# Optimization experiments

Hardware: AMD Instinct MI355X
Metric: run time of the kernel (lower is better)

## Reference

```python
import jax, jax.numpy as jnp
import numpy as np

N = 65536          # total nodes across batch
C = 256            # in channels
COUT = 256         # out channels
B = 8              # batch size (graphs)
EMB = 512          # emb channels
N_EDGE_TYPE = 7
N_NODE_TYPE = 7
AVG_DEGREE = 7
E = N * AVG_DEGREE
GROUP = 32         # min(32, channels)
EPS = 1e-5


def setup_inputs() -> dict:
    key = jax.random.key(0)
    ks = jax.random.split(key, 10)
    # GraphConv init: uniform xavier-like with fan scaled by avg_degree
    std = (2.0 / float(AVG_DEGREE * C + AVG_DEGREE * COUT)) ** 0.5
    a = (3.0 ** 0.5) * std
    return {
        "x": jax.random.normal(ks[0], (N, C), jnp.float32),
        "emb": jax.random.normal(ks[1], (B, EMB), jnp.float32),
        "batch_id": jnp.sort(jax.random.randint(ks[2], (N,), 0, B, jnp.int32)),
        "edge_index": jax.random.randint(ks[3], (2, E), 0, N, jnp.int32),
        "edge_type": jax.random.randint(ks[4], (E,), 0, N_EDGE_TYPE, jnp.int32),
        "node_type": jax.random.randint(ks[5], (N,), 0, N_NODE_TYPE, jnp.int32),
        "gn1_w": jnp.ones((1, C), jnp.float32),
        "gn1_b": jnp.zeros((1, C), jnp.float32),
        "conv1_w": jax.random.uniform(ks[6], (N_EDGE_TYPE * (C + N_NODE_TYPE), COUT), jnp.float32, -a, a),
        "emb_w": jax.random.normal(ks[7], (EMB, COUT), jnp.float32) * 0.02,
        "emb_b": jnp.zeros((COUT,), jnp.float32),
        "gn2_w": jnp.ones((1, COUT), jnp.float32),
        "gn2_b": jnp.zeros((1, COUT), jnp.float32),
        "conv2_w": jax.random.uniform(ks[8], (N_EDGE_TYPE * (COUT + N_NODE_TYPE), COUT), jnp.float32, -a, a),
    }


def _adjust_for_group(t, cpg):
    # sum stats within each group of cpg channels, broadcast back: [B, C]
    if cpg > 1:
        Bsz, Cn = t.shape
        g = Cn // cpg
        t = t.reshape(Bsz, g, cpg).sum(-1, keepdims=True)
        t = jnp.broadcast_to(t, (Bsz, g, cpg)).reshape(Bsz, Cn)
    return t


def dual_octree_group_norm(data, batch_id, w, b):
    # data: [N, C]; per-graph group norm via segment sums
    Cn = data.shape[1]
    cpg = Cn // GROUP
    ones = jnp.ones((data.shape[0], 1), data.dtype)
    count = jax.ops.segment_sum(ones, batch_id, num_segments=B) * cpg   # [B,1]
    inv_count = 1.0 / (count + EPS)
    mean = jax.ops.segment_sum(data, batch_id, num_segments=B) * inv_count
    mean = _adjust_for_group(mean, cpg)
    out = data - mean[batch_id]
    var = jax.ops.segment_sum(out * out, batch_id, num_segments=B) * inv_count
    var = _adjust_for_group(var, cpg)
    inv_std = 1.0 / jnp.sqrt(var + EPS)
    out = out * inv_std[batch_id]
    return out * w + b


def graph_conv(x, weights, edge_index, edge_type, node_type):
    # concat one-hot node type channels
    one_hot = jax.nn.one_hot(node_type, N_NODE_TYPE, dtype=x.dtype)
    xa = jnp.concatenate([x, one_hot], axis=1)          # [N, C+T]
    row, col = edge_index[0], edge_index[1]
    index = row * N_EDGE_TYPE + edge_type               # [E]
    col_data = jax.ops.segment_sum(xa[col], index, num_segments=xa.shape[0] * N_EDGE_TYPE)
    return col_data.reshape(xa.shape[0], -1) @ weights  # [N, COUT]


def reference(x, emb, batch_id, edge_index, edge_type, node_type,
              gn1_w, gn1_b, conv1_w, emb_w, emb_b, gn2_w, gn2_b, conv2_w):
    h = dual_octree_group_norm(x, batch_id, gn1_w, gn1_b)
    h = jax.nn.silu(h)
    h = graph_conv(h, conv1_w, edge_index, edge_type, node_type)
    emb_out = jax.nn.silu(emb) @ emb_w + emb_b          # [B, COUT]
    h = h + emb_out[batch_id]                           # per-batch add (loop in torch)
    h = dual_octree_group_norm(h, batch_id, gn2_w, gn2_b)
    h = jax.nn.silu(h)                                  # dropout p=0 -> identity
    h = graph_conv(h, conv2_w, edge_index, edge_type, node_type)
    return x + h                                        # skip is Identity (Cout==C)
```

## Files before the change

kernel.cpp:

```cpp
#include <hip/hip_runtime.h>
#include <math.h>

#define N_NODES 65536
#define B_GR    8
#define EMB_N   512
#define E_EDGES 458752
#define NSEG    458752
#define TSTRIDE 288
#define GK      2016
#define EPS     1e-5f

typedef unsigned short u16;
typedef unsigned int   u32;
typedef __bf16 bf16x8 __attribute__((ext_vector_type(8)));
typedef float  f32x4  __attribute__((ext_vector_type(4)));
typedef u16    u16x8  __attribute__((ext_vector_type(8)));

__device__ __forceinline__ float bf2f(u16 u) {
    u32 x = ((u32)u) << 16; float f; __builtin_memcpy(&f, &x, 4); return f;
}
__device__ __forceinline__ u16 f2bf(float f) {
    u32 x; __builtin_memcpy(&x, &f, 4);
    u32 r = x + 0x7fffu + ((x >> 16) & 1u);
    return (u16)(r >> 16);
}

#define SW(row, k8) ((k8) ^ (((row) >> 1) & 3))

__global__ __launch_bounds__(256) void zero_kernel(int* __restrict__ hist,
                                                   float* __restrict__ S, float* __restrict__ Q) {
    int i = blockIdx.x * 256 + threadIdx.x;
    if (i < NSEG) hist[i] = 0;
    if (i < 2048) { S[i] = 0.f; Q[i] = 0.f; }
}
__global__ __launch_bounds__(256) void zero_sq_kernel(float* __restrict__ S, float* __restrict__ Q) {
    int i = blockIdx.x * 256 + threadIdx.x;
    if (i < 2048) { S[i] = 0.f; Q[i] = 0.f; }
}

__global__ __launch_bounds__(256) void prep_kernel(
    const float* __restrict__ w1, const float* __restrict__ w2,
    u16* __restrict__ Wt1, u16* __restrict__ Wt2,
    const float* __restrict__ emb, const float* __restrict__ embw,
    const float* __restrict__ embb, float* __restrict__ embout)
{
    int bid = blockIdx.x, tid = threadIdx.x;
    if (bid < 4032) {
        const float* Win = (bid < 2016) ? w1 : w2;
        u16* Wt = (bid < 2016) ? Wt1 : Wt2;
        int idx = (bid % 2016) * 256 + tid;
        int n = idx / GK;
        int k = idx - n * GK;
        int t = k / TSTRIDE;
        int c = k - t * TSTRIDE;
        u16 v = (c < 263) ? f2bf(Win[(size_t)(t * 263 + c) * 256 + n]) : (u16)0;
        Wt[idx] = v;
    } else {
        __shared__ float semb[B_GR * EMB_N];
        for (int i = tid; i < B_GR * EMB_N; i += 256) {
            float e = emb[i];
            semb[i] = e / (1.f + expf(-e));
        }
        __syncthreads();
        float acc[8];
        float bb = embb[tid];
#pragma unroll
        for (int b = 0; b < 8; b++) acc[b] = bb;
        for (int k = 0; k < EMB_N; k++) {
            float wv = embw[k * 256 + tid];
#pragma unroll
            for (int b = 0; b < 8; b++) acc[b] += semb[b * EMB_N + k] * wv;
        }
#pragma unroll
        for (int b = 0; b < 8; b++) embout[b * 256 + tid] = acc[b];
    }
}

__global__ __launch_bounds__(256) void stats_kernel(const float* __restrict__ xin,
                                                    const int* __restrict__ batch_id,
                                                    float* __restrict__ S, float* __restrict__ Q) {
    int c = threadIdx.x;
    int n0 = blockIdx.x * 64;
    float s = 0.f, q = 0.f;
    int bcur = batch_id[n0];
    for (int r = 0; r < 64; r++) {
        int n = n0 + r;
        int b = batch_id[n];
        if (b != bcur) {
            atomicAdd(&S[bcur * 256 + c], s);
            atomicAdd(&Q[bcur * 256 + c], q);
            s = 0.f; q = 0.f; bcur = b;
        }
        float v = xin[(size_t)n * 256 + c];
        s += v;
        q = fmaf(v, v, q);
    }
    atomicAdd(&S[bcur * 256 + c], s);
    atomicAdd(&Q[bcur * 256 + c], q);
}

__global__ __launch_bounds__(256) void finalize_kernel(const int* __restrict__ batch_id,
                                                       const float* __restrict__ S, const float* __restrict__ Q,
                                                       float* __restrict__ gmean, float* __restrict__ gistd) {
    __shared__ int scnt[8];
    int tid = threadIdx.x;
    if (tid < 8) scnt[tid] = 0;
    __syncthreads();
    int c0=0,c1=0,c2=0,c3=0,c4=0,c5=0,c6=0,c7=0;
    for (int i = tid; i < N_NODES; i += 256) {
        int b = batch_id[i];
        c0 += (b==0); c1 += (b==1); c2 += (b==2); c3 += (b==3);
        c4 += (b==4); c5 += (b==5); c6 += (b==6); c7 += (b==7);
    }
    atomicAdd(&scnt[0], c0); atomicAdd(&scnt[1], c1); atomicAdd(&scnt[2], c2); atomicAdd(&scnt[3], c3);
    atomicAdd(&scnt[4], c4); atomicAdd(&scnt[5], c5); atomicAdd(&scnt[6], c6); atomicAdd(&scnt[7], c7);
    __syncthreads();
    int b = tid >> 5, g = tid & 31;
    float Sg = 0.f, Qg = 0.f;
#pragma unroll
    for (int k = 0; k < 8; k++) {
        Sg += S[b * 256 + g * 8 + k];
        Qg += Q[b * 256 + g * 8 + k];
    }
    float cnt8 = (float)scnt[b] * 8.f;
    float D = cnt8 + EPS;
    float m = Sg / D;
    float var = (Qg - 2.f * m * Sg + cnt8 * m * m) / D;
    float istd = rsqrtf(var + EPS);
    gmean[tid] = m;
    gistd[tid] = istd;
}

__global__ __launch_bounds__(256) void norm_silu_kernel(const float* __restrict__ xin,
                                                        const int* __restrict__ batch_id,
                                                        const float* __restrict__ gmean, const float* __restrict__ gistd,
                                                        const float* __restrict__ w, const float* __restrict__ bias,
                                                        u16* __restrict__ yout) {
    int tid = threadIdx.x;
    int n = blockIdx.x * 8 + (tid >> 5);
    int g = tid & 31;
    int c0 = g * 8;
    int b = batch_id[n];
    float m = gmean[b * 32 + g], is = gistd[b * 32 + g];
    u16x8 o;
#pragma unroll
    for (int k = 0; k < 8; k++) {
        float v = (xin[(size_t)n * 256 + c0 + k] - m) * is;
        v = v * w[c0 + k] + bias[c0 + k];
        v = v / (1.f + expf(-v));
        o[k] = f2bf(v);
    }
    *(u16x8*)&yout[(size_t)n * 256 + c0] = o;
}

__global__ __launch_bounds__(256) void hist_kernel(const int* __restrict__ ei, const int* __restrict__ et,
                                                   int* __restrict__ hist) {
    int e = blockIdx.x * 256 + threadIdx.x;
    if (e >= E_EDGES) return;
    int s = ei[e] * 7 + et[e];
    atomicAdd(&hist[s], 1);
}

__global__ __launch_bounds__(512) void scan1_kernel(const int* __restrict__ hist, int* __restrict__ partials) {
    __shared__ int sd[512];
    int i = blockIdx.x * 512 + threadIdx.x;
    sd[threadIdx.x] = hist[i];
    __syncthreads();
    for (int off = 256; off > 0; off >>= 1) {
        if (threadIdx.x < off) sd[threadIdx.x] += sd[threadIdx.x + off];
        __syncthreads();
    }
    if (threadIdx.x == 0) partials[blockIdx.x] = sd[0];
}

__global__ __launch_bounds__(1024) void scan2_kernel(int* __restrict__ partials) {
    __shared__ int sd[1024];
    int t = threadIdx.x;
    int v = (t < 896) ? partials[t] : 0;
    sd[t] = v;
    __syncthreads();
    for (int off = 1; off < 1024; off <<= 1) {
        int u = (t >= off) ? sd[t - off] : 0;
        __syncthreads();
        sd[t] += u;
        __syncthreads();
    }
    if (t < 896) partials[t] = sd[t] - v;
}

__global__ __launch_bounds__(512) void scan3_kernel(int* __restrict__ hist_offs, const int* __restrict__ partials,
                                                    int* __restrict__ cursor) {
    __shared__ int sd[512];
    int t = threadIdx.x;
    int i = blockIdx.x * 512 + t;
    int c = hist_offs[i];
    sd[t] = c;
    __syncthreads();
    for (int off = 1; off < 512; off <<= 1) {
        int u = (t >= off) ? sd[t - off] : 0;
        __syncthreads();
        sd[t] += u;
        __syncthreads();
    }
    int o = partials[blockIdx.x] + sd[t] - c;
    hist_offs[i] = o;
    cursor[i] = o;
}

__global__ __launch_bounds__(256) void fill_kernel(const int* __restrict__ ei, const int* __restrict__ et,
                                                   int* __restrict__ cursor, int* __restrict__ elist) {
    int e = blockIdx.x * 256 + threadIdx.x;
    if (e >= E_EDGES) return;
    int s = ei[e] * 7 + et[e];
    int p = atomicAdd(&cursor[s], 1);
    if (p >= 0 && p < E_EDGES) elist[p] = ei[E_EDGES + e];
}

__global__ __launch_bounds__(256) void gemm_fused_kernel(
    const u16* __restrict__ y, const u16* __restrict__ Bt,
    const int* __restrict__ offs, const int* __restrict__ cursor,
    const int* __restrict__ elist, const int* __restrict__ node_type,
    const int* __restrict__ batch_id, const float* __restrict__ embout,
    const float* __restrict__ xres, float* __restrict__ out, int mode)
{
    __shared__ __align__(16) u16 As[64 * 32];
    __shared__ __align__(16) u16 Bs[256 * 32];
    int tid = threadIdx.x;
    int lane = tid & 63;
    int wn = tid >> 6;
    int lm = lane & 15, lq = lane >> 4;
    int m0 = blockIdx.x * 64;
    int ar = tid >> 2, aq = tid & 3;

    f32x4 acc[4][4];
    f32x4 zz = {0.f, 0.f, 0.f, 0.f};
#pragma unroll
    for (int i = 0; i < 4; i++)
#pragma unroll
        for (int j = 0; j < 4; j++) acc[i][j] = zz;

    const u16* btp = Bt + (size_t)ar * GK + aq * 8;

    float a8[8];
    u16x8 breg[4];

    for (int t = 0; t < 7; t++) {
        int s = (m0 + ar) * 7 + t;
        int st = offs[s], en = cursor[s];
        int cnt = en - st;
        int col[4];
#pragma unroll
        for (int u = 0; u < 4; u++) col[u] = (cnt > u) ? elist[st + u] : -1;

#pragma unroll
        for (int j = 0; j < 8; j++) a8[j] = 0.f;
        {
            int cb = aq * 8;
#pragma unroll
            for (int u = 0; u < 4; u++)
                if (col[u] >= 0) {
                    u16x8 v = *(const u16x8*)&y[(size_t)col[u] * 256 + cb];
#pragma unroll
                    for (int j = 0; j < 8; j++) a8[j] += bf2f(v[j]);
                }
            if (cnt > 4)
                for (int e = st + 4; e < en; e++) {
                    u16x8 v = *(const u16x8*)&y[(size_t)elist[e] * 256 + cb];
#pragma unroll
                    for (int j = 0; j < 8; j++) a8[j] += bf2f(v[j]);
                }
        }
        {
            int kb = t * TSTRIDE;
#pragma unroll
            for (int i2 = 0; i2 < 4; i2++) breg[i2] = *(const u16x8*)&btp[(size_t)i2 * 64 * GK + kb];
        }

#pragma unroll
        for (int c9 = 0; c9 < 9; c9++) {
            __syncthreads();
            u16x8 o;
#pragma unroll
            for (int j = 0; j < 8; j++) o[j] = f2bf(a8[j]);
            *(u16x8*)&As[ar * 32 + SW(ar, aq) * 8] = o;
#pragma unroll
            for (int i2 = 0; i2 < 4; i2++) {
                int row = ar + i2 * 64;
                *(u16x8*)&Bs[row * 32 + SW(row, aq) * 8] = breg[i2];
            }
            __syncthreads();
            bf16x8 a[4], b[4];
#pragma unroll
            for (int i = 0; i < 4; i++) {
                int ra = i * 16 + lm;
                a[i] = *(const bf16x8*)&As[ra * 32 + SW(ra, lq) * 8];
            }
#pragma unroll
            for (int j = 0; j < 4; j++) {
                int rb = wn * 64 + j * 16 + lm;
                b[j] = *(const bf16x8*)&Bs[rb * 32 + SW(rb, lq) * 8];
            }
            u16x8 gv[4];
            int nt4[4];
#pragma unroll
            for (int j = 0; j < 8; j++) a8[j] = 0.f;
            if (c9 < 7) {
                int cb = (c9 + 1) * 32 + aq * 8;
#pragma unroll
                for (int u = 0; u < 4; u++)
                    if (col[u] >= 0) gv[u] = *(const u16x8*)&y[(size_t)col[u] * 256 + cb];
                int kb = t * TSTRIDE + (c9 + 1) * 32;
#pragma unroll
                for (int i2 = 0; i2 < 4; i2++) breg[i2] = *(const u16x8*)&btp[(size_t)i2 * 64 * GK + kb];
            } else if (c9 == 7) {
                if (aq == 0) {
#pragma unroll
                    for (int u = 0; u < 4; u++)
                        if (col[u] >= 0) nt4[u] = node_type[col[u]];
                }
                int kb = t * TSTRIDE + 8 * 32;
#pragma unroll
                for (int i2 = 0; i2 < 4; i2++) breg[i2] = *(const u16x8*)&btp[(size_t)i2 * 64 * GK + kb];
            }
#pragma unroll
            for (int i = 0; i < 4; i++)
#pragma unroll
                for (int j = 0; j < 4; j++)
                    acc[i][j] = __builtin_amdgcn_mfma_f32_16x16x32_bf16(a[i], b[j], acc[i][j], 0, 0, 0);
            if (c9 < 7) {
#pragma unroll
                for (int u = 0; u < 4; u++)
                    if (col[u] >= 0) {
#pragma unroll
                        for (int j = 0; j < 8; j++) a8[j] += bf2f(gv[u][j]);
                    }
                if (cnt > 4) {
                    int cb = (c9 + 1) * 32 + aq * 8;
                    for (int e = st + 4; e < en; e++) {
                        u16x8 v = *(const u16x8*)&y[(size_t)elist[e] * 256 + cb];
#pragma unroll
                        for (int j = 0; j < 8; j++) a8[j] += bf2f(v[j]);
                    }
                }
            } else if (c9 == 7) {
                if (aq == 0) {
#pragma unroll
                    for (int u = 0; u < 4; u++)
                        if (col[u] >= 0) {
#pragma unroll
                            for (int j = 0; j < 7; j++) a8[j] += (nt4[u] == j) ? 1.f : 0.f;
                        }
                    if (cnt > 4)
                        for (int e = st + 4; e < en; e++) {
                            int nt = node_type[elist[e]];
#pragma unroll
                            for (int j = 0; j < 7; j++) a8[j] += (nt == j) ? 1.f : 0.f;
                        }
                }
            }
        }
    }

#pragma unroll
    for (int i = 0; i < 4; i++) {
#pragma unroll
        for (int r = 0; r < 4; r++) {
            size_t m = (size_t)m0 + i * 16 + lq * 4 + r;
            float addv[4];
            if (mode == 0) {
                int b = batch_id[m];
#pragma unroll
                for (int j = 0; j < 4; j++) addv[j] = embout[b * 256 + wn * 64 + j * 16 + lm];
            } else {
#pragma unroll
                for (int j = 0; j < 4; j++) addv[j] = xres[m * 256 + wn * 64 + j * 16 + lm];
            }
#pragma unroll
            for (int j = 0; j < 4; j++) {
                int n = wn * 64 + j * 16 + lm;
                out[m * 256 + n] = acc[i][j][r] + addv[j];
            }
        }
    }
}

extern "C" void kernel_launch(void* const* d_in, const int* in_sizes, int n_in,
                              void* d_out, int out_size, void* d_ws, size_t ws_size,
                              hipStream_t stream) {
    const float* x    = (const float*)d_in[0];
    const float* emb  = (const float*)d_in[1];
    const int* bid    = (const int*)d_in[2];
    const int* ei     = (const int*)d_in[3];
    const int* et     = (const int*)d_in[4];
    const int* ntp    = (const int*)d_in[5];
    const float* gn1w = (const float*)d_in[6];
    const float* gn1b = (const float*)d_in[7];
    const float* w1   = (const float*)d_in[8];
    const float* embw = (const float*)d_in[9];
    const float* embb = (const float*)d_in[10];
    const float* gn2w = (const float*)d_in[11];
    const float* gn2b = (const float*)d_in[12];
    const float* w2   = (const float*)d_in[13];
    float* out = (float*)d_out;

    char* p = (char*)d_ws;
    size_t off = 0;
    auto nxt = [&](size_t bytes) -> void* {
        void* r = p + off;
        off += (bytes + 255) & ~(size_t)255;
        return r;
    };
    u16*   y       = (u16*)nxt((size_t)N_NODES * 256 * 2);
    u16*   Wt1     = (u16*)nxt((size_t)256 * GK * 2);
    u16*   Wt2     = (u16*)nxt((size_t)256 * GK * 2);
    float* embout  = (float*)nxt(8 * 256 * 4);
    float* S       = (float*)nxt(2048 * 4);
    float* Q       = (float*)nxt(2048 * 4);
    float* gmean   = (float*)nxt(256 * 4);
    float* gistd   = (float*)nxt(256 * 4);
    int*   offs    = (int*)nxt((size_t)NSEG * 4);
    int*   cursor  = (int*)nxt((size_t)NSEG * 4);
    int*   parts   = (int*)nxt(1024 * 4);
    int*   elist   = (int*)nxt((size_t)E_EDGES * 4);
    float* h2      = out;
    (void)ws_size; (void)in_sizes; (void)n_in; (void)out_size;

    zero_kernel<<<1792, 256, 0, stream>>>(offs, S, Q);
    prep_kernel<<<4033, 256, 0, stream>>>(w1, w2, Wt1, Wt2, emb, embw, embb, embout);
    stats_kernel<<<1024, 256, 0, stream>>>(x, bid, S, Q);
    finalize_kernel<<<1, 256, 0, stream>>>(bid, S, Q, gmean, gistd);
    norm_silu_kernel<<<8192, 256, 0, stream>>>(x, bid, gmean, gistd, gn1w, gn1b, y);
    hist_kernel<<<1792, 256, 0, stream>>>(ei, et, offs);
    scan1_kernel<<<896, 512, 0, stream>>>(offs, parts);
    scan2_kernel<<<1, 1024, 0, stream>>>(parts);
    scan3_kernel<<<896, 512, 0, stream>>>(offs, parts, cursor);
    fill_kernel<<<1792, 256, 0, stream>>>(ei, et, cursor, elist);
    gemm_fused_kernel<<<1024, 256, 0, stream>>>(y, Wt1, offs, cursor, elist, ntp, bid, embout, x, h2, 0);
    zero_sq_kernel<<<8, 256, 0, stream>>>(S, Q);
    stats_kernel<<<1024, 256, 0, stream>>>(h2, bid, S, Q);
    finalize_kernel<<<1, 256, 0, stream>>>(bid, S, Q, gmean, gistd);
    norm_silu_kernel<<<8192, 256, 0, stream>>>(h2, bid, gmean, gistd, gn2w, gn2b, y);
    gemm_fused_kernel<<<1024, 256, 0, stream>>>(y, Wt2, offs, cursor, elist, ntp, bid, embout, x, out, 1);
}
```

Before: 831.2 us.

## Restructure fused gather-GEMM with 512 threads, double-buffered A, register-direct B

The fused gather+GEMM kernel moves to 512 threads. Each pair of threads splits a segment's edge gather and combines the halves with a shuffle. The A tile is double-buffered in LDS so each k-step needs one barrier, and B fragments are loaded straight from global memory into registers instead of staged through LDS. The next edge type's gather is prefetched during the last k-step, and MFMA issue gets raised priority. Separately, the weight transpose uses a coalesced LDS tile, per-graph counts come from a dedicated ballot kernel rather than a single-block loop, and the S/Q zeroing is folded into finalize. In exchange, B reads from global memory are less reused, the kernel needs more registers per thread, and the control flow is more complex.

After: 720.1 us. 1.15x faster.

```diff
diff --git a/kernel.cpp b/kernel.cpp
--- a/kernel.cpp
+++ b/kernel.cpp
@@ -28,14 +28,24 @@
 #define SW(row, k8) ((k8) ^ (((row) >> 1) & 3))
 
 __global__ __launch_bounds__(256) void zero_kernel(int* __restrict__ hist,
-                                                   float* __restrict__ S, float* __restrict__ Q) {
+                                                   float* __restrict__ S, float* __restrict__ Q,
+                                                   int* __restrict__ cnt) {
     int i = blockIdx.x * 256 + threadIdx.x;
     if (i < NSEG) hist[i] = 0;
     if (i < 2048) { S[i] = 0.f; Q[i] = 0.f; }
-}
-__global__ __launch_bounds__(256) void zero_sq_kernel(float* __restrict__ S, float* __restrict__ Q) {
+    if (i < 8) cnt[i] = 0;
+}
+
+__global__ __launch_bounds__(256) void count_kernel(const int* __restrict__ batch_id,
+                                                    int* __restrict__ cnt) {
     int i = blockIdx.x * 256 + threadIdx.x;
-    if (i < 2048) { S[i] = 0.f; Q[i] = 0.f; }
+    int b = batch_id[i];
+#pragma unroll
+    for (int bb = 0; bb < 8; bb++) {
+        unsigned long long m = __ballot(b == bb);
+        if ((threadIdx.x & 63) == 0 && m)
+            atomicAdd(&cnt[bb], (int)__popcll(m));
+    }
 }
 
 __global__ __launch_bounds__(256) void prep_kernel(
@@ -45,16 +55,29 @@
     const float* __restrict__ embb, float* __restrict__ embout)
 {
     int bid = blockIdx.x, tid = threadIdx.x;
-    if (bid < 4032) {
-        const float* Win = (bid < 2016) ? w1 : w2;
-        u16* Wt = (bid < 2016) ? Wt1 : Wt2;
-        int idx = (bid % 2016) * 256 + tid;
-        int n = idx / GK;
-        int k = idx - n * GK;
-        int t = k / TSTRIDE;
-        int c = k - t * TSTRIDE;
-        u16 v = (c < 263) ? f2bf(Win[(size_t)(t * 263 + c) * 256 + n]) : (u16)0;
-        Wt[idx] = v;
+    if (bid < 1008) {
+        const float* Win = (bid < 504) ? w1 : w2;
+        u16* Wt = (bid < 504) ? Wt1 : Wt2;
+        int r  = bid % 504;
+        int t  = r / 72;
+        int r2 = r % 72;
+        int c0 = (r2 / 8) * 32;
+        int n0 = (r2 % 8) * 32;
+        __shared__ float tile[32][33];
+        int cl = tid & 31, rh = tid >> 5;
+#pragma unroll
+        for (int rr = 0; rr < 4; rr++) {
+            int c = c0 + rh + rr * 8;
+            float v = 0.f;
+            if (c < 263) v = Win[(size_t)(t * 263 + c) * 256 + n0 + cl];
+            tile[rh + rr * 8][cl] = v;
+        }
+        __syncthreads();
+#pragma unroll
+        for (int rr = 0; rr < 4; rr++) {
+            int n = n0 + rh + rr * 8;
+            Wt[(size_t)n * GK + t * TSTRIDE + c0 + cl] = f2bf(tile[cl][rh + rr * 8]);
+        }
     } else {
         __shared__ float semb[B_GR * EMB_N];
         for (int i = tid; i < B_GR * EMB_N; i += 256) {
@@ -99,30 +122,21 @@
     atomicAdd(&Q[bcur * 256 + c], q);
 }
 
-__global__ __launch_bounds__(256) void finalize_kernel(const int* __restrict__ batch_id,
-                                                       const float* __restrict__ S, const float* __restrict__ Q,
+__global__ __launch_bounds__(256) void finalize_kernel(const int* __restrict__ cnt,
+                                                       float* __restrict__ S, float* __restrict__ Q,
                                                        float* __restrict__ gmean, float* __restrict__ gistd) {
-    __shared__ int scnt[8];
     int tid = threadIdx.x;
-    if (tid < 8) scnt[tid] = 0;
-    __syncthreads();
-    int c0=0,c1=0,c2=0,c3=0,c4=0,c5=0,c6=0,c7=0;
-    for (int i = tid; i < N_NODES; i += 256) {
-        int b = batch_id[i];
-        c0 += (b==0); c1 += (b==1); c2 += (b==2); c3 += (b==3);
-        c4 += (b==4); c5 += (b==5); c6 += (b==6); c7 += (b==7);
-    }
-    atomicAdd(&scnt[0], c0); atomicAdd(&scnt[1], c1); atomicAdd(&scnt[2], c2); atomicAdd(&scnt[3], c3);
-    atomicAdd(&scnt[4], c4); atomicAdd(&scnt[5], c5); atomicAdd(&scnt[6], c6); atomicAdd(&scnt[7], c7);
-    __syncthreads();
     int b = tid >> 5, g = tid & 31;
     float Sg = 0.f, Qg = 0.f;
 #pragma unroll
     for (int k = 0; k < 8; k++) {
-        Sg += S[b * 256 + g * 8 + k];
-        Qg += Q[b * 256 + g * 8 + k];
-    }
-    float cnt8 = (float)scnt[b] * 8.f;
+        int idx = b * 256 + g * 8 + k;
+        Sg += S[idx];
+        Qg += Q[idx];
+        S[idx] = 0.f;
+        Q[idx] = 0.f;
+    }
+    float cnt8 = (float)cnt[b] * 8.f;
     float D = cnt8 + EPS;
     float m = Sg / D;
     float var = (Qg - 2.f * m * Sg + cnt8 * m * m) / D;
@@ -216,127 +230,140 @@
     if (p >= 0 && p < E_EDGES) elist[p] = ei[E_EDGES + e];
 }
 
-__global__ __launch_bounds__(256) void gemm_fused_kernel(
+__global__ __launch_bounds__(512, 4) void gemm_fused_kernel(
     const u16* __restrict__ y, const u16* __restrict__ Bt,
     const int* __restrict__ offs, const int* __restrict__ cursor,
     const int* __restrict__ elist, const int* __restrict__ node_type,
     const int* __restrict__ batch_id, const float* __restrict__ embout,
     const float* __restrict__ xres, float* __restrict__ out, int mode)
 {
-    __shared__ __align__(16) u16 As[64 * 32];
-    __shared__ __align__(16) u16 Bs[256 * 32];
+    __shared__ __align__(16) u16 As[2][64 * 32];
     int tid = threadIdx.x;
     int lane = tid & 63;
     int wn = tid >> 6;
     int lm = lane & 15, lq = lane >> 4;
     int m0 = blockIdx.x * 64;
-    int ar = tid >> 2, aq = tid & 3;
-
-    f32x4 acc[4][4];
+    int ar = tid >> 3;
+    int aq = (tid >> 1) & 3;
+    int half = tid & 1;
+
+    f32x4 acc[4][2];
     f32x4 zz = {0.f, 0.f, 0.f, 0.f};
 #pragma unroll
     for (int i = 0; i < 4; i++)
 #pragma unroll
-        for (int j = 0; j < 4; j++) acc[i][j] = zz;
-
-    const u16* btp = Bt + (size_t)ar * GK + aq * 8;
+        for (int j = 0; j < 2; j++) acc[i][j] = zz;
+
+    const u16* btp0 = Bt + (size_t)(wn * 32 + lm) * GK + lq * 8;
+    const u16* btp1 = btp0 + (size_t)16 * GK;
+
+    int sbase = (m0 + ar) * 7;
+    int st = offs[sbase], en = cursor[sbase];
+    int col[2];
+    col[0] = (st + half     < en) ? elist[st + half]     : -1;
+    col[1] = (st + half + 2 < en) ? elist[st + half + 2] : -1;
 
     float a8[8];
-    u16x8 breg[4];
+#pragma unroll
+    for (int j = 0; j < 8; j++) a8[j] = 0.f;
+#pragma unroll
+    for (int u = 0; u < 2; u++)
+        if (col[u] >= 0) {
+            u16x8 v = *(const u16x8*)&y[(size_t)col[u] * 256 + aq * 8];
+#pragma unroll
+            for (int j = 0; j < 8; j++) a8[j] += bf2f(v[j]);
+        }
+    if (en - st > 4)
+        for (int e = st + 4 + half; e < en; e += 2) {
+            u16x8 v = *(const u16x8*)&y[(size_t)elist[e] * 256 + aq * 8];
+#pragma unroll
+            for (int j = 0; j < 8; j++) a8[j] += bf2f(v[j]);
+        }
+
+    bf16x8 bcur[2], bnxt[2];
+    bcur[0] = *(const bf16x8*)&btp0[0];
+    bcur[1] = *(const bf16x8*)&btp1[0];
+
+    int st_n = 0, en_n = 0;
+    int coln[2] = {-1, -1};
+    int buf = 0;
 
     for (int t = 0; t < 7; t++) {
-        int s = (m0 + ar) * 7 + t;
-        int st = offs[s], en = cursor[s];
-        int cnt = en - st;
-        int col[4];
-#pragma unroll
-        for (int u = 0; u < 4; u++) col[u] = (cnt > u) ? elist[st + u] : -1;
-
-#pragma unroll
-        for (int j = 0; j < 8; j++) a8[j] = 0.f;
-        {
-            int cb = aq * 8;
-#pragma unroll
-            for (int u = 0; u < 4; u++)
-                if (col[u] >= 0) {
-                    u16x8 v = *(const u16x8*)&y[(size_t)col[u] * 256 + cb];
-#pragma unroll
-                    for (int j = 0; j < 8; j++) a8[j] += bf2f(v[j]);
-                }
-            if (cnt > 4)
-                for (int e = st + 4; e < en; e++) {
-                    u16x8 v = *(const u16x8*)&y[(size_t)elist[e] * 256 + cb];
-#pragma unroll
-                    for (int j = 0; j < 8; j++) a8[j] += bf2f(v[j]);
-                }
-        }
-        {
-            int kb = t * TSTRIDE;
-#pragma unroll
-            for (int i2 = 0; i2 < 4; i2++) breg[i2] = *(const u16x8*)&btp[(size_t)i2 * 64 * GK + kb];
-        }
-
 #pragma unroll
         for (int c9 = 0; c9 < 9; c9++) {
+#pragma unroll
+            for (int j = 0; j < 8; j++) a8[j] += __shfl_xor(a8[j], 1);
+            if (half == 0) {
+                u16x8 o;
+#pragma unroll
+                for (int j = 0; j < 8; j++) o[j] = f2bf(a8[j]);
+                *(u16x8*)&As[buf][ar * 32 + SW(ar, aq) * 8] = o;
+            }
             __syncthreads();
-            u16x8 o;
-#pragma unroll
-            for (int j = 0; j < 8; j++) o[j] = f2bf(a8[j]);
-            *(u16x8*)&As[ar * 32 + SW(ar, aq) * 8] = o;
-#pragma unroll
-            for (int i2 = 0; i2 < 4; i2++) {
-                int row = ar + i2 * 64;
-                *(u16x8*)&Bs[row * 32 + SW(row, aq) * 8] = breg[i2];
-            }
-            __syncthreads();
-            bf16x8 a[4], b[4];
+            bf16x8 a[4];
 #pragma unroll
             for (int i = 0; i < 4; i++) {
                 int ra = i * 16 + lm;
-                a[i] = *(const bf16x8*)&As[ra * 32 + SW(ra, lq) * 8];
-            }
-#pragma unroll
-            for (int j = 0; j < 4; j++) {
-                int rb = wn * 64 + j * 16 + lm;
-                b[j] = *(const bf16x8*)&Bs[rb * 32 + SW(rb, lq) * 8];
-            }
-            u16x8 gv[4];
-            int nt4[4];
+                a[i] = *(const bf16x8*)&As[buf][ra * 32 + SW(ra, lq) * 8];
+            }
+            u16x8 gv[2];
+            int nt2[2];
 #pragma unroll
             for (int j = 0; j < 8; j++) a8[j] = 0.f;
             if (c9 < 7) {
                 int cb = (c9 + 1) * 32 + aq * 8;
 #pragma unroll
-                for (int u = 0; u < 4; u++)
+                for (int u = 0; u < 2; u++)
                     if (col[u] >= 0) gv[u] = *(const u16x8*)&y[(size_t)col[u] * 256 + cb];
                 int kb = t * TSTRIDE + (c9 + 1) * 32;
-#pragma unroll
-                for (int i2 = 0; i2 < 4; i2++) breg[i2] = *(const u16x8*)&btp[(size_t)i2 * 64 * GK + kb];
+                bnxt[0] = *(const bf16x8*)&btp0[kb];
+                bnxt[1] = *(const bf16x8*)&btp1[kb];
+                if (c9 == 6 && t < 6) {
+                    int sn = sbase + t + 1;
+                    st_n = offs[sn];
+                    en_n = cursor[sn];
+                }
             } else if (c9 == 7) {
                 if (aq == 0) {
 #pragma unroll
-                    for (int u = 0; u < 4; u++)
-                        if (col[u] >= 0) nt4[u] = node_type[col[u]];
-                }
-                int kb = t * TSTRIDE + 8 * 32;
-#pragma unroll
-                for (int i2 = 0; i2 < 4; i2++) breg[i2] = *(const u16x8*)&btp[(size_t)i2 * 64 * GK + kb];
-            }
+                    for (int u = 0; u < 2; u++)
+                        nt2[u] = (col[u] >= 0) ? node_type[col[u]] : -1;
+                }
+                int kb = t * TSTRIDE + 256;
+                bnxt[0] = *(const bf16x8*)&btp0[kb];
+                bnxt[1] = *(const bf16x8*)&btp1[kb];
+                if (t < 6) {
+                    coln[0] = (st_n + half     < en_n) ? elist[st_n + half]     : -1;
+                    coln[1] = (st_n + half + 2 < en_n) ? elist[st_n + half + 2] : -1;
+                }
+            } else {
+                if (t < 6) {
+                    int cb = aq * 8;
+#pragma unroll
+                    for (int u = 0; u < 2; u++)
+                        if (coln[u] >= 0) gv[u] = *(const u16x8*)&y[(size_t)coln[u] * 256 + cb];
+                    int kb = (t + 1) * TSTRIDE;
+                    bnxt[0] = *(const bf16x8*)&btp0[kb];
+                    bnxt[1] = *(const bf16x8*)&btp1[kb];
+                }
+            }
+            __builtin_amdgcn_s_setprio(1);
 #pragma unroll
             for (int i = 0; i < 4; i++)
 #pragma unroll
-                for (int j = 0; j < 4; j++)
-                    acc[i][j] = __builtin_amdgcn_mfma_f32_16x16x32_bf16(a[i], b[j], acc[i][j], 0, 0, 0);
+                for (int j = 0; j < 2; j++)
+                    acc[i][j] = __builtin_amdgcn_mfma_f32_16x16x32_bf16(a[i], bcur[j], acc[i][j], 0, 0, 0);
+            __builtin_amdgcn_s_setprio(0);
             if (c9 < 7) {
 #pragma unroll
-                for (int u = 0; u < 4; u++)
+                for (int u = 0; u < 2; u++)
                     if (col[u] >= 0) {
 #pragma unroll
                         for (int j = 0; j < 8; j++) a8[j] += bf2f(gv[u][j]);
                     }
-                if (cnt > 4) {
+                if (en - st > 4) {
                     int cb = (c9 + 1) * 32 + aq * 8;
-                    for (int e = st + 4; e < en; e++) {
+                    for (int e = st + 4 + half; e < en; e += 2) {
                         u16x8 v = *(const u16x8*)&y[(size_t)elist[e] * 256 + cb];
 #pragma unroll
                         for (int j = 0; j < 8; j++) a8[j] += bf2f(v[j]);
@@ -345,19 +372,38 @@
             } else if (c9 == 7) {
                 if (aq == 0) {
 #pragma unroll
-                    for (int u = 0; u < 4; u++)
+                    for (int u = 0; u < 2; u++)
                         if (col[u] >= 0) {
 #pragma unroll
-                            for (int j = 0; j < 7; j++) a8[j] += (nt4[u] == j) ? 1.f : 0.f;
+                            for (int j = 0; j < 7; j++) a8[j] += (nt2[u] == j) ? 1.f : 0.f;
                         }
-                    if (cnt > 4)
-                        for (int e = st + 4; e < en; e++) {
+                    if (en - st > 4)
+                        for (int e = st + 4 + half; e < en; e += 2) {
                             int nt = node_type[elist[e]];
 #pragma unroll
                             for (int j = 0; j < 7; j++) a8[j] += (nt == j) ? 1.f : 0.f;
                         }
                 }
-            }
+            } else {
+                if (t < 6) {
+#pragma unroll
+                    for (int u = 0; u < 2; u++)
+                        if (coln[u] >= 0) {
+#pragma unroll
+                            for (int j = 0; j < 8; j++) a8[j] += bf2f(gv[u][j]);
+                        }
+                    if (en_n - st_n > 4)
+                        for (int e = st_n + 4 + half; e < en_n; e += 2) {
+                            u16x8 v = *(const u16x8*)&y[(size_t)elist[e] * 256 + aq * 8];
+#pragma unroll
+                            for (int j = 0; j < 8; j++) a8[j] += bf2f(v[j]);
+                        }
+                    col[0] = coln[0]; col[1] = coln[1];
+                    st = st_n; en = en_n;
+                }
+            }
+            bcur[0] = bnxt[0]; bcur[1] = bnxt[1];
+            buf ^= 1;
         }
     }
 
@@ -366,18 +412,18 @@
 #pragma unroll
         for (int r = 0; r < 4; r++) {
             size_t m = (size_t)m0 + i * 16 + lq * 4 + r;
-            float addv[4];
+            float addv[2];
             if (mode == 0) {
                 int b = batch_id[m];
 #pragma unroll
-                for (int j = 0; j < 4; j++) addv[j] = embout[b * 256 + wn * 64 + j * 16 + lm];
+                for (int j = 0; j < 2; j++) addv[j] = embout[b * 256 + wn * 32 + j * 16 + lm];
             } else {
 #pragma unroll
-                for (int j = 0; j < 4; j++) addv[j] = xres[m * 256 + wn * 64 + j * 16 + lm];
-            }
-#pragma unroll
-            for (int j = 0; j < 4; j++) {
-                int n = wn * 64 + j * 16 + lm;
+                for (int j = 0; j < 2; j++) addv[j] = xres[m * 256 + wn * 32 + j * 16 + lm];
+            }
+#pragma unroll
+            for (int j = 0; j < 2; j++) {
+                int n = wn * 32 + j * 16 + lm;
                 out[m * 256 + n] = acc[i][j][r] + addv[j];
             }
         }
@@ -418,6 +464,7 @@
     float* Q       = (float*)nxt(2048 * 4);
     float* gmean   = (float*)nxt(256 * 4);
     float* gistd   = (float*)nxt(256 * 4);
+    int*   cnt     = (int*)nxt(8 * 4);
     int*   offs    = (int*)nxt((size_t)NSEG * 4);
     int*   cursor  = (int*)nxt((size_t)NSEG * 4);
     int*   parts   = (int*)nxt(1024 * 4);
@@ -425,20 +472,20 @@
     float* h2      = out;
     (void)ws_size; (void)in_sizes; (void)n_in; (void)out_size;
 
-    zero_kernel<<<1792, 256, 0, stream>>>(offs, S, Q);
-    prep_kernel<<<4033, 256, 0, stream>>>(w1, w2, Wt1, Wt2, emb, embw, embb, embout);
+    zero_kernel<<<1792, 256, 0, stream>>>(offs, S, Q, cnt);
+    count_kernel<<<256, 256, 0, stream>>>(bid, cnt);
+    prep_kernel<<<1009, 256, 0, stream>>>(w1, w2, Wt1, Wt2, emb, embw, embb, embout);
     stats_kernel<<<1024, 256, 0, stream>>>(x, bid, S, Q);
-    finalize_kernel<<<1, 256, 0, stream>>>(bid, S, Q, gmean, gistd);
+    finalize_kernel<<<1, 256, 0, stream>>>(cnt, S, Q, gmean, gistd);
     norm_silu_kernel<<<8192, 256, 0, stream>>>(x, bid, gmean, gistd, gn1w, gn1b, y);
     hist_kernel<<<1792, 256, 0, stream>>>(ei, et, offs);
     scan1_kernel<<<896, 512, 0, stream>>>(offs, parts);
     scan2_kernel<<<1, 1024, 0, stream>>>(parts);
     scan3_kernel<<<896, 512, 0, stream>>>(offs, parts, cursor);
     fill_kernel<<<1792, 256, 0, stream>>>(ei, et, cursor, elist);
-    gemm_fused_kernel<<<1024, 256, 0, stream>>>(y, Wt1, offs, cursor, elist, ntp, bid, embout, x, h2, 0);
-    zero_sq_kernel<<<8, 256, 0, stream>>>(S, Q);
+    gemm_fused_kernel<<<1024, 512, 0, stream>>>(y, Wt1, offs, cursor, elist, ntp, bid, embout, x, h2, 0);
     stats_kernel<<<1024, 256, 0, stream>>>(h2, bid, S, Q);
-    finalize_kernel<<<1, 256, 0, stream>>>(bid, S, Q, gmean, gistd);
+    finalize_kernel<<<1, 256, 0, stream>>>(cnt, S, Q, gmean, gistd);
     norm_silu_kernel<<<8192, 256, 0, stream>>>(h2, bid, gmean, gistd, gn2w, gn2b, y);
-    gemm_fused_kernel<<<1024, 256, 0, stream>>>(y, Wt2, offs, cursor, elist, ntp, bid, embout, x, out, 1);
-}
+    gemm_fused_kernel<<<1024, 512, 0, stream>>>(y, Wt2, offs, cursor, elist, ntp, bid, embout, x, out, 1);
+}
```
